# Kernel optimization log

Measured on AMD Instinct MI355X. Metric: run time of the kernel, lower is better.

## Reference

```python
import jax, jax.numpy as jnp
import numpy as np

N_NODES = 100000
N_EDGES = 1600000
IN_F = 256
OUT_F = 128


def setup_inputs() -> dict:
    key = jax.random.key(0)
    k1, k2, k3, k4, k5, k6 = jax.random.split(key, 6)
    x = jax.random.normal(k1, (N_NODES, IN_F), dtype=jnp.float32)
    stdv = 1.0 / np.sqrt(OUT_F)
    weight = jax.random.uniform(k2, (IN_F, OUT_F), dtype=jnp.float32, minval=-stdv, maxval=stdv)
    bias = jax.random.uniform(k3, (OUT_F,), dtype=jnp.float32, minval=-stdv, maxval=stdv)
    edge_src = jax.random.randint(k4, (N_EDGES,), 0, N_NODES, dtype=jnp.int32)
    edge_dst = jnp.sort(jax.random.randint(k5, (N_EDGES,), 0, N_NODES, dtype=jnp.int32))
    edge_val = jax.random.uniform(k6, (N_EDGES,), dtype=jnp.float32)
    return {"x": x, "weight": weight, "bias": bias,
            "edge_src": edge_src, "edge_dst": edge_dst, "edge_val": edge_val}


def reference(x, weight, bias, edge_src, edge_dst, edge_val):
    # support = X @ W   (dense GEMM, [N, out_f])
    support = x @ weight
    # output = A @ support, A sparse COO: out[dst] += val * support[src]
    msgs = support[edge_src] * edge_val[:, None]          # [E, out_f]
    output = jax.ops.segment_sum(msgs, edge_dst, num_segments=N_NODES,
                                 indices_are_sorted=True)  # [N, out_f]
    return jnp.tanh(output + bias)
```

## Files before the change

kernel.cpp:

```cpp
#include <hip/hip_runtime.h>
#include <hip/hip_bf16.h>

typedef _Float16 f16;
typedef f16 f16x8 __attribute__((ext_vector_type(8)));
typedef f16 f16x4 __attribute__((ext_vector_type(4)));
typedef float f32x4 __attribute__((ext_vector_type(4)));

#define IN_F 256
#define OUT_F 128
#define BK 64
#define BM 64

__global__ __launch_bounds__(256) void prep_w(const float* __restrict__ W,
                                              f16* __restrict__ Wt) {
    int i = blockIdx.x * 256 + threadIdx.x;
    int k = i >> 7;
    int n = i & 127;
    Wt[n * IN_F + k] = (f16)W[i];
}

__global__ __launch_bounds__(256) void seg_bounds(const int* __restrict__ dst,
                                                  int* __restrict__ rs,
                                                  int* __restrict__ re, int E) {
    int i = blockIdx.x * 256 + threadIdx.x;
    if (i >= E) return;
    int d = dst[i];
    if (i == 0 || dst[i - 1] != d) rs[d] = i;
    if (i == E - 1 || dst[i + 1] != d) re[d] = i + 1;
}

__global__ __launch_bounds__(256) void gemm_xw(const float* __restrict__ X,
                                               const f16* __restrict__ Wt,
                                               f16* __restrict__ S, int M) {
    __shared__ f16 sx[2][BM * BK] __attribute__((aligned(16)));

    const int w   = threadIdx.x >> 6;
    const int l   = threadIdx.x & 63;
    const int r   = l & 15;
    const int khi = l >> 4;
    const int wm = w >> 1, wn = w & 1;
    const int brow  = blockIdx.x * BM;
    const int mbase = wm * 32;
    const int nbase = wn * 64;

    const int srow = w * 16 + (l >> 4);
    const int scol = (l & 15) * 4;

    f32x4 acc[2][4] = {};
    float4 xv[4];
    f16x8 bcur[4], bnxt[4];

    #pragma unroll
    for (int j = 0; j < 4; ++j) {
        int rloc = srow + j * 4;
        int rg = brow + rloc; rg = rg < M ? rg : M - 1;
        xv[j] = *(const float4*)(X + (size_t)rg * IN_F + scol);
    }
    #pragma unroll
    for (int n = 0; n < 4; ++n)
        bcur[n] = *(const f16x8*)(Wt + (size_t)(nbase + n * 16 + r) * IN_F + khi * 8);
    #pragma unroll
    for (int j = 0; j < 4; ++j) {
        int rloc = srow + j * 4;
        f16x4 hv = { (f16)xv[j].x, (f16)xv[j].y, (f16)xv[j].z, (f16)xv[j].w };
        *(f16x4*)&sx[0][rloc * BK + (scol ^ ((rloc & 7) << 3))] = hv;
    }
    __syncthreads();

    #pragma unroll
    for (int t = 0; t < 4; ++t) {
        if (t < 3) {
            const int k0 = (t + 1) * BK;
            #pragma unroll
            for (int j = 0; j < 4; ++j) {
                int rloc = srow + j * 4;
                int rg = brow + rloc; rg = rg < M ? rg : M - 1;
                xv[j] = *(const float4*)(X + (size_t)rg * IN_F + k0 + scol);
            }
        }
        #pragma unroll
        for (int kk = 0; kk < 2; ++kk) {
            const int nk = t * 2 + kk + 1;
            if (nk < 8) {
                const int kg = (nk >> 1) * BK + (nk & 1) * 32 + khi * 8;
                #pragma unroll
                for (int n = 0; n < 4; ++n)
                    bnxt[n] = *(const f16x8*)(Wt + (size_t)(nbase + n * 16 + r) * IN_F + kg);
            }
            f16x8 a[2];
            const int sidx = (kk * 32 + khi * 8) ^ ((r & 7) << 3);
            #pragma unroll
            for (int m = 0; m < 2; ++m) {
                int arow = mbase + m * 16 + r;
                a[m] = *(const f16x8*)&sx[t & 1][arow * BK + sidx];
            }
            #pragma unroll
            for (int m = 0; m < 2; ++m)
                #pragma unroll
                for (int n = 0; n < 4; ++n)
                    acc[m][n] = __builtin_amdgcn_mfma_f32_16x16x32_f16(a[m], bcur[n], acc[m][n], 0, 0, 0);
            #pragma unroll
            for (int n = 0; n < 4; ++n) bcur[n] = bnxt[n];
        }
        if (t < 3) {
            #pragma unroll
            for (int j = 0; j < 4; ++j) {
                int rloc = srow + j * 4;
                f16x4 hv = { (f16)xv[j].x, (f16)xv[j].y, (f16)xv[j].z, (f16)xv[j].w };
                *(f16x4*)&sx[(t + 1) & 1][rloc * BK + (scol ^ ((rloc & 7) << 3))] = hv;
            }
        }
        __syncthreads();
    }

    #pragma unroll
    for (int m = 0; m < 2; ++m) {
        int row0 = brow + mbase + m * 16 + khi * 4;
        #pragma unroll
        for (int i = 0; i < 4; ++i) {
            int row = row0 + i;
            if (row < M) {
                #pragma unroll
                for (int n = 0; n < 4; ++n)
                    S[(size_t)row * OUT_F + nbase + n * 16 + r] = (f16)acc[m][n][i];
            }
        }
    }
}

__global__ __launch_bounds__(256) void aggregate(const f16* __restrict__ S,
                                                 const int* __restrict__ rs,
                                                 const int* __restrict__ re,
                                                 const int* __restrict__ esrc,
                                                 const float* __restrict__ eval,
                                                 const float* __restrict__ bias,
                                                 float* __restrict__ out, int N) {
    const int wave = threadIdx.x >> 6;
    const int lane = threadIdx.x & 63;
    const int node = blockIdx.x * 4 + wave;
    if (node >= N) return;

    const int g = lane >> 4;
    const int p = lane & 15;

    const int s = rs[node];
    const int e = re[node];

    float acc[8] = {};

    for (int base = s; base < e; base += 16) {
        int   se[4];
        float ve[4];
        #pragma unroll
        for (int j = 0; j < 4; ++j) {
            int ei  = base + j * 4 + g;
            int eic = min(ei, e - 1);
            se[j] = esrc[eic];
            ve[j] = eval[eic];
            if (ei >= e) ve[j] = 0.f;
        }
        f16x8 h[4];
        #pragma unroll
        for (int j = 0; j < 4; ++j)
            h[j] = *(const f16x8*)(S + (size_t)se[j] * OUT_F + p * 8);
        #pragma unroll
        for (int j = 0; j < 4; ++j)
            #pragma unroll
            for (int q = 0; q < 8; ++q)
                acc[q] += ve[j] * (float)h[j][q];
    }

    #pragma unroll
    for (int q = 0; q < 8; ++q) {
        acc[q] += __shfl_xor(acc[q], 16);
        acc[q] += __shfl_xor(acc[q], 32);
    }

    if (lane < 32) {
        const int half = lane >> 4;
        const int f0 = 8 * p + 4 * half;
        float4 bb = *(const float4*)(bias + f0);
        float4 o;
        o.x = tanhf(acc[4 * half + 0] + bb.x);
        o.y = tanhf(acc[4 * half + 1] + bb.y);
        o.z = tanhf(acc[4 * half + 2] + bb.z);
        o.w = tanhf(acc[4 * half + 3] + bb.w);
        *(float4*)(out + (size_t)node * OUT_F + f0) = o;
    }
}

extern "C" void kernel_launch(void* const* d_in, const int* in_sizes, int n_in,
                              void* d_out, int out_size, void* d_ws, size_t ws_size,
                              hipStream_t stream) {
    const float* X    = (const float*)d_in[0];
    const float* W    = (const float*)d_in[1];
    const float* bias = (const float*)d_in[2];
    const int*   esrc = (const int*)d_in[3];
    const int*   edst = (const int*)d_in[4];
    const float* eval = (const float*)d_in[5];
    float* out = (float*)d_out;

    const int N = in_sizes[0] / IN_F;
    const int E = in_sizes[3];

    char* ws = (char*)d_ws;
    f16* Wt = (f16*)ws;
    f16* S  = (f16*)(ws + 65536);
    int* rs = (int*)(ws + 65536 + (size_t)N * OUT_F * 2);
    int* re = rs + N;

    hipMemsetAsync(rs, 0, 2 * (size_t)N * sizeof(int), stream);
    prep_w<<<(IN_F * OUT_F) / 256, 256, 0, stream>>>(W, Wt);
    seg_bounds<<<(E + 255) / 256, 256, 0, stream>>>(edst, rs, re, E);
    gemm_xw<<<(N + BM - 1) / BM, 256, 0, stream>>>(X, Wt, S, N);
    aggregate<<<(N + 3) / 4, 256, 0, stream>>>(S, rs, re, esrc, eval, bias, out, N);
}
```

Measured before the change: 116.3 us.

## Fuse prep kernels, drop memset, stage full X tile in LDS

The memset, weight-transpose and segment-bounds kernels are merged into a single prep kernel. That kernel writes empty-segment bounds itself, so the separate memset is no longer needed. The GEMM now loads the whole 64x256 X tile into LDS at once, with an XOR swizzle across 16 rows, instead of double-buffering 64-column slices. It also adds a 4-blocks-per-CU launch bound. This removes two launches and the per-slice barriers, but uses 32KB of LDS per block and gives up overlapping X loads with MFMA work.

New measurement: 109.3 us, median of 2. 1.06x faster.

```diff
diff --git a/kernel.cpp b/kernel.cpp
--- a/kernel.cpp
+++ b/kernel.cpp
@@ -8,31 +8,44 @@
 
 #define IN_F 256
 #define OUT_F 128
-#define BK 64
 #define BM 64
 
-__global__ __launch_bounds__(256) void prep_w(const float* __restrict__ W,
-                                              f16* __restrict__ Wt) {
+__global__ __launch_bounds__(256) void prep(const float* __restrict__ W,
+                                            f16* __restrict__ Wt,
+                                            const int* __restrict__ dst,
+                                            int* __restrict__ rs,
+                                            int* __restrict__ re,
+                                            int E, int N) {
     int i = blockIdx.x * 256 + threadIdx.x;
-    int k = i >> 7;
-    int n = i & 127;
-    Wt[n * IN_F + k] = (f16)W[i];
-}
-
-__global__ __launch_bounds__(256) void seg_bounds(const int* __restrict__ dst,
-                                                  int* __restrict__ rs,
-                                                  int* __restrict__ re, int E) {
-    int i = blockIdx.x * 256 + threadIdx.x;
-    if (i >= E) return;
-    int d = dst[i];
-    if (i == 0 || dst[i - 1] != d) rs[d] = i;
-    if (i == E - 1 || dst[i + 1] != d) re[d] = i + 1;
-}
-
-__global__ __launch_bounds__(256) void gemm_xw(const float* __restrict__ X,
-                                               const f16* __restrict__ Wt,
-                                               f16* __restrict__ S, int M) {
-    __shared__ f16 sx[2][BM * BK] __attribute__((aligned(16)));
+    if (i < IN_F * OUT_F) {
+        int k = i >> 7;
+        int n = i & 127;
+        Wt[n * IN_F + k] = (f16)W[i];
+    }
+    if (i < E) {
+        int d = dst[i];
+        if (i == 0) {
+            rs[d] = 0;
+            for (int v = 0; v < d; ++v) { rs[v] = 0; re[v] = 0; }
+        } else {
+            int a = dst[i - 1];
+            if (a != d) {
+                re[a] = i;
+                rs[d] = i;
+                for (int v = a + 1; v < d; ++v) { rs[v] = i; re[v] = i; }
+            }
+        }
+        if (i == E - 1) {
+            re[d] = E;
+            for (int v = d + 1; v < N; ++v) { rs[v] = E; re[v] = E; }
+        }
+    }
+}
+
+__global__ __launch_bounds__(256, 4) void gemm_xw(const float* __restrict__ X,
+                                                  const f16* __restrict__ Wt,
+                                                  f16* __restrict__ S, int M) {
+    __shared__ f16 sx[BM * IN_F] __attribute__((aligned(16)));
 
     const int w   = threadIdx.x >> 6;
     const int l   = threadIdx.x & 63;
@@ -43,74 +56,53 @@
     const int mbase = wm * 32;
     const int nbase = wn * 64;
 
-    const int srow = w * 16 + (l >> 4);
-    const int scol = (l & 15) * 4;
-
     f32x4 acc[2][4] = {};
-    float4 xv[4];
     f16x8 bcur[4], bnxt[4];
 
-    #pragma unroll
-    for (int j = 0; j < 4; ++j) {
-        int rloc = srow + j * 4;
-        int rg = brow + rloc; rg = rg < M ? rg : M - 1;
-        xv[j] = *(const float4*)(X + (size_t)rg * IN_F + scol);
-    }
     #pragma unroll
     for (int n = 0; n < 4; ++n)
         bcur[n] = *(const f16x8*)(Wt + (size_t)(nbase + n * 16 + r) * IN_F + khi * 8);
-    #pragma unroll
-    for (int j = 0; j < 4; ++j) {
-        int rloc = srow + j * 4;
-        f16x4 hv = { (f16)xv[j].x, (f16)xv[j].y, (f16)xv[j].z, (f16)xv[j].w };
-        *(f16x4*)&sx[0][rloc * BK + (scol ^ ((rloc & 7) << 3))] = hv;
+
+    #pragma unroll
+    for (int jr = 0; jr < 4; ++jr) {
+        const int rloc = w * 16 + jr * 4 + (l >> 4);
+        int rg = brow + rloc; rg = rg < M ? rg : M - 1;
+        const float* xp = X + (size_t)rg * IN_F + (l & 15) * 4;
+        float4 xv[4];
+        #pragma unroll
+        for (int jc = 0; jc < 4; ++jc)
+            xv[jc] = *(const float4*)(xp + jc * 64);
+        #pragma unroll
+        for (int jc = 0; jc < 4; ++jc) {
+            f16x4 hv = { (f16)xv[jc].x, (f16)xv[jc].y, (f16)xv[jc].z, (f16)xv[jc].w };
+            const int cf16 = (jc * 64 + (l & 15) * 4) ^ ((rloc & 15) << 3);
+            *(f16x4*)&sx[rloc * IN_F + cf16] = hv;
+        }
     }
     __syncthreads();
 
     #pragma unroll
-    for (int t = 0; t < 4; ++t) {
-        if (t < 3) {
-            const int k0 = (t + 1) * BK;
+    for (int kk = 0; kk < 8; ++kk) {
+        if (kk < 7) {
+            const int kg = (kk + 1) * 32 + khi * 8;
             #pragma unroll
-            for (int j = 0; j < 4; ++j) {
-                int rloc = srow + j * 4;
-                int rg = brow + rloc; rg = rg < M ? rg : M - 1;
-                xv[j] = *(const float4*)(X + (size_t)rg * IN_F + k0 + scol);
-            }
-        }
-        #pragma unroll
-        for (int kk = 0; kk < 2; ++kk) {
-            const int nk = t * 2 + kk + 1;
-            if (nk < 8) {
-                const int kg = (nk >> 1) * BK + (nk & 1) * 32 + khi * 8;
-                #pragma unroll
-                for (int n = 0; n < 4; ++n)
-                    bnxt[n] = *(const f16x8*)(Wt + (size_t)(nbase + n * 16 + r) * IN_F + kg);
-            }
-            f16x8 a[2];
-            const int sidx = (kk * 32 + khi * 8) ^ ((r & 7) << 3);
+            for (int n = 0; n < 4; ++n)
+                bnxt[n] = *(const f16x8*)(Wt + (size_t)(nbase + n * 16 + r) * IN_F + kg);
+        }
+        f16x8 a[2];
+        #pragma unroll
+        for (int m = 0; m < 2; ++m) {
+            const int arow = mbase + m * 16 + r;
+            const int cf16 = (kk * 32 + khi * 8) ^ (r << 3);
+            a[m] = *(const f16x8*)&sx[arow * IN_F + cf16];
+        }
+        #pragma unroll
+        for (int m = 0; m < 2; ++m)
             #pragma unroll
-            for (int m = 0; m < 2; ++m) {
-                int arow = mbase + m * 16 + r;
-                a[m] = *(const f16x8*)&sx[t & 1][arow * BK + sidx];
-            }
-            #pragma unroll
-            for (int m = 0; m < 2; ++m)
-                #pragma unroll
-                for (int n = 0; n < 4; ++n)
-                    acc[m][n] = __builtin_amdgcn_mfma_f32_16x16x32_f16(a[m], bcur[n], acc[m][n], 0, 0, 0);
-            #pragma unroll
-            for (int n = 0; n < 4; ++n) bcur[n] = bnxt[n];
-        }
-        if (t < 3) {
-            #pragma unroll
-            for (int j = 0; j < 4; ++j) {
-                int rloc = srow + j * 4;
-                f16x4 hv = { (f16)xv[j].x, (f16)xv[j].y, (f16)xv[j].z, (f16)xv[j].w };
-                *(f16x4*)&sx[(t + 1) & 1][rloc * BK + (scol ^ ((rloc & 7) << 3))] = hv;
-            }
-        }
-        __syncthreads();
+            for (int n = 0; n < 4; ++n)
+                acc[m][n] = __builtin_amdgcn_mfma_f32_16x16x32_f16(a[m], bcur[n], acc[m][n], 0, 0, 0);
+        #pragma unroll
+        for (int n = 0; n < 4; ++n) bcur[n] = bnxt[n];
     }
 
     #pragma unroll
@@ -209,9 +201,7 @@
     int* rs = (int*)(ws + 65536 + (size_t)N * OUT_F * 2);
     int* re = rs + N;
 
-    hipMemsetAsync(rs, 0, 2 * (size_t)N * sizeof(int), stream);
-    prep_w<<<(IN_F * OUT_F) / 256, 256, 0, stream>>>(W, Wt);
-    seg_bounds<<<(E + 255) / 256, 256, 0, stream>>>(edst, rs, re, E);
+    prep<<<(E + 255) / 256, 256, 0, stream>>>(W, Wt, edst, rs, re, E, N);
     gemm_xw<<<(N + BM - 1) / BM, 256, 0, stream>>>(X, Wt, S, N);
     aggregate<<<(N + 3) / 4, 256, 0, stream>>>(S, rs, re, esrc, eval, bias, out, N);
 }
```
